# Optimization experiments

Hardware: AMD Instinct MI355X
Metric: run time of the kernel (lower is better)

Reference implementation:

```python
import jax, jax.numpy as jnp
import numpy as np

N = 100_000      # nodes
E = 1_600_000    # edges (avg degree 16)
H = 128          # hidden_channels == num_node_features
L = 6            # SAGEConv layers (third=True)
G = 128          # graphs in batch (for global_mean_pool)
C = 10           # num_classes
EPS = 1e-5       # BatchNorm eps


def setup_inputs() -> dict:
    key = jax.random.key(0)
    ks = jax.random.split(key, 8)
    s = 1.0 / np.sqrt(H)
    x = jax.random.normal(ks[0], (N, H), jnp.float32)
    edge_index = jax.random.randint(ks[1], (2, E), 0, N, dtype=jnp.int32)
    batch = jnp.sort(jax.random.randint(ks[2], (N,), 0, G, dtype=jnp.int32))
    return {
        "x": x,
        "edge_index": edge_index,
        "batch": batch,
        "Wl": jax.random.normal(ks[3], (L, H, H), jnp.float32) * s,  # neighbor lin
        "bl": jnp.zeros((L, H), jnp.float32),
        "Wr": jax.random.normal(ks[4], (L, H, H), jnp.float32) * s,  # root lin (no bias)
        "gamma": jnp.ones((L, H), jnp.float32),
        "beta": jnp.zeros((L, H), jnp.float32),
        "lin_W": jax.random.normal(ks[5], (H, C), jnp.float32) * s,
        "lin_b": jnp.zeros((C,), jnp.float32),
    }


def reference(x, edge_index, batch, Wl, bl, Wr, gamma, beta, lin_W, lin_b):
    src, dst = edge_index[0], edge_index[1]
    n = x.shape[0]
    # in-degree for mean aggregation (constant across layers)
    deg = jax.ops.segment_sum(jnp.ones((src.shape[0],), x.dtype), dst, num_segments=n)
    inv_deg = jnp.where(deg > 0, 1.0 / deg, 0.0)[:, None]  # [n,1]

    for l in range(Wl.shape[0]):
        # SAGEConv: lin_l(mean_{j->i} x_j) + lin_r(x_i)
        agg = jax.ops.segment_sum(x[src], dst, num_segments=n) * inv_deg  # [n,H]
        h = agg @ Wl[l] + bl[l] + x @ Wr[l]
        # BatchNorm1d (training-style batch stats, biased variance)
        mu = jnp.mean(h, axis=0)
        var = jnp.mean((h - mu) ** 2, axis=0)
        h = (h - mu) * jax.lax.rsqrt(var + EPS) * gamma[l] + beta[l]
        x = jax.nn.relu(h)

    # global_mean_pool over graph ids
    cnt = jax.ops.segment_sum(jnp.ones((n,), x.dtype), batch, num_segments=G)
    pooled = jax.ops.segment_sum(x, batch, num_segments=G) / jnp.maximum(cnt, 1.0)[:, None]
    # dropout(p=0.5) is identity in eval mode
    return pooled @ lin_W + lin_b  # [G, C]
```

## Files before the change

kernel.cpp:

```cpp
#include <hip/hip_runtime.h>
#include <hip/hip_bf16.h>

#define N_NODES 100000
#define N_EDGES 1600000
#define HDIM    128
#define NLAYER  6
#define NGRAPH  128
#define NCLASS  10
#define BN_EPS  1e-5f

#define POOL_SPLIT 16

#define NBUCK   196
#define BSH     9
#define KC_BLOCKS 250
#define KC_CHUNK  6400
#define LCOL_CAP  10240

#define GBM 128
#define NBLK_G ((N_NODES + GBM - 1) / GBM)

typedef __attribute__((ext_vector_type(8))) short short8v;
typedef __attribute__((ext_vector_type(4))) float f32x4;
typedef __attribute__((ext_vector_type(2))) float f32x2;
typedef __attribute__((ext_vector_type(4))) int int4v;
typedef __attribute__((ext_vector_type(2))) int int2v;

__device__ __forceinline__ float b2f(unsigned short h) {
    return __uint_as_float(((unsigned int)h) << 16);
}
__device__ __forceinline__ unsigned short f2b(float f) {
    unsigned int u = __float_as_uint(f);
    u += 0x7FFF + ((u >> 16) & 1);
    return (unsigned short)(u >> 16);
}
__device__ __forceinline__ void gl_lds16(const void* g, void* l) {
    __builtin_amdgcn_global_load_lds((const __attribute__((address_space(1))) unsigned int*)g,
                                     (__attribute__((address_space(3))) unsigned int*)l,
                                     16, 0, 0);
}
__device__ __forceinline__ short8v bn_pack(short8v v, float4 scA, float4 scB,
                                           float4 shA, float4 shB) {
    short8v o;
    o[0] = (short)f2b(fmaxf(0.f, b2f((unsigned short)v[0]) * scA.x + shA.x));
    o[1] = (short)f2b(fmaxf(0.f, b2f((unsigned short)v[1]) * scA.y + shA.y));
    o[2] = (short)f2b(fmaxf(0.f, b2f((unsigned short)v[2]) * scA.z + shA.z));
    o[3] = (short)f2b(fmaxf(0.f, b2f((unsigned short)v[3]) * scA.w + shA.w));
    o[4] = (short)f2b(fmaxf(0.f, b2f((unsigned short)v[4]) * scB.x + shB.x));
    o[5] = (short)f2b(fmaxf(0.f, b2f((unsigned short)v[5]) * scB.y + shB.y));
    o[6] = (short)f2b(fmaxf(0.f, b2f((unsigned short)v[6]) * scB.z + shB.z));
    o[7] = (short)f2b(fmaxf(0.f, b2f((unsigned short)v[7]) * scB.w + shB.w));
    return o;
}


__global__ void __launch_bounds__(256) k_hist(const int* __restrict__ dst,
                                              int* __restrict__ bcnt) {
    __shared__ int h[NBUCK];
    for (int i = threadIdx.x; i < NBUCK; i += 256) h[i] = 0;
    __syncthreads();
    const int4v* d4 = (const int4v*)dst;
    int base = blockIdx.x * (KC_CHUNK / 4);
    for (int i = threadIdx.x; i < KC_CHUNK / 4; i += 256) {
        int4v d = __builtin_nontemporal_load(d4 + base + i);
        atomicAdd(&h[d[0] >> BSH], 1);
        atomicAdd(&h[d[1] >> BSH], 1);
        atomicAdd(&h[d[2] >> BSH], 1);
        atomicAdd(&h[d[3] >> BSH], 1);
    }
    __syncthreads();
    for (int i = threadIdx.x; i < NBUCK; i += 256)
        if (h[i]) atomicAdd(&bcnt[i], h[i]);
}

__global__ void k_bscan(const int* __restrict__ bcnt, int* __restrict__ boff,
                        int* __restrict__ bcur, int* __restrict__ row_off) {
    if (threadIdx.x == 0 && blockIdx.x == 0) {
        int acc = 0;
        for (int i = 0; i < NBUCK; ++i) {
            boff[i] = acc; bcur[i] = acc; acc += bcnt[i];
        }
        boff[NBUCK] = acc;
        row_off[N_NODES] = N_EDGES;
    }
}

__global__ void __launch_bounds__(256) k_part(const int* __restrict__ src,
                                              const int* __restrict__ dst,
                                              int* __restrict__ bcur,
                                              int2v* __restrict__ P) {
    __shared__ int h[NBUCK];
    __shared__ int gbase[NBUCK];
    for (int i = threadIdx.x; i < NBUCK; i += 256) h[i] = 0;
    __syncthreads();
    const int4v* d4 = (const int4v*)dst;
    const int4v* s4 = (const int4v*)src;
    const int base = blockIdx.x * (KC_CHUNK / 4);
    for (int i = threadIdx.x; i < KC_CHUNK / 4; i += 256) {
        int4v d = __builtin_nontemporal_load(d4 + base + i);
        atomicAdd(&h[d[0] >> BSH], 1);
        atomicAdd(&h[d[1] >> BSH], 1);
        atomicAdd(&h[d[2] >> BSH], 1);
        atomicAdd(&h[d[3] >> BSH], 1);
    }
    __syncthreads();
    for (int i = threadIdx.x; i < NBUCK; i += 256) {
        int c = h[i];
        gbase[i] = c ? atomicAdd(&bcur[i], c) : 0;
        h[i] = 0;
    }
    __syncthreads();
    for (int i = threadIdx.x; i < KC_CHUNK / 4; i += 256) {
        int4v d = __builtin_nontemporal_load(d4 + base + i);
        int4v s = __builtin_nontemporal_load(s4 + base + i);
#pragma unroll
        for (int k = 0; k < 4; ++k) {
            int b = d[k] >> BSH;
            int pos = gbase[b] + atomicAdd(&h[b], 1);
            int2v pr; pr[0] = s[k]; pr[1] = d[k];
            P[pos] = pr;
        }
    }
}

__global__ void __launch_bounds__(1024) k_bucket(const int2v* __restrict__ P,
                                                 const int* __restrict__ boff,
                                                 int* __restrict__ row_off,
                                                 int* __restrict__ col) {
    __shared__ int ldeg[512];
    __shared__ int lcur[512];
    __shared__ int lcol[LCOL_CAP];
    const int tid = threadIdx.x;
    const int b = blockIdx.x;
    const int pbeg = boff[b], pend = boff[b + 1];
    const int nE = pend - pbeg;
    const int n0 = b << BSH;
    if (tid < 512) ldeg[tid] = 0;
    __syncthreads();
    for (int i = tid; i < nE; i += 1024) {
        int2v pr = P[pbeg + i];
        atomicAdd(&ldeg[pr[1] - n0], 1);
    }
    __syncthreads();
    int myd = (tid < 512) ? ldeg[tid] : 0;
    for (int off = 1; off < 512; off <<= 1) {
        int t = 0;
        if (tid < 512 && tid >= off) t = ldeg[tid - off];
        __syncthreads();
        if (tid < 512) ldeg[tid] += t;
        __syncthreads();
    }
    if (tid < 512) {
        int excl = ldeg[tid] - myd;
        lcur[tid] = excl;
        int node = n0 + tid;
        if (node < N_NODES) row_off[node] = pbeg + excl;
    }
    __syncthreads();
    for (int i = tid; i < nE; i += 1024) {
        int2v pr = P[pbeg + i];
        int pos = atomicAdd(&lcur[pr[1] - n0], 1);
        if (pos < LCOL_CAP) lcol[pos] = pr[0];
    }
    __syncthreads();
    for (int i = tid; i < nE; i += 1024) col[pbeg + i] = lcol[i];
}


__global__ void __launch_bounds__(256) k_cvt_x(const float* __restrict__ x,
                                               unsigned short* __restrict__ Xb,
                                               unsigned int* __restrict__ X8) {
    int idx = blockIdx.x * 256 + threadIdx.x;
    f32x4 v = __builtin_nontemporal_load(((const f32x4*)x) + idx);
    ushort4 o = { f2b(v[0]), f2b(v[1]), f2b(v[2]), f2b(v[3]) };
    ((ushort4*)Xb)[idx] = o;
    unsigned int d = 0;
    d = __builtin_amdgcn_cvt_pk_fp8_f32(v[0], v[1], d, false);
    d = __builtin_amdgcn_cvt_pk_fp8_f32(v[2], v[3], d, true);
    X8[idx] = d;
}

__global__ void __launch_bounds__(256) k_cvt_w(const float* __restrict__ Wl,
                                               const float* __restrict__ Wr,
                                               unsigned short* __restrict__ Wtb) {
    int idx = blockIdx.x * 256 + threadIdx.x;
    int kk = idx & 255;
    int n  = (idx >> 8) & 127;
    int l  = idx >> 15;
    float v = (kk < HDIM) ? Wl[l * HDIM * HDIM + kk * HDIM + n]
                          : Wr[l * HDIM * HDIM + (kk - HDIM) * HDIM + n];
    Wtb[idx] = f2b(v);
}

__global__ void __launch_bounds__(256) k_bnx8(const unsigned short* __restrict__ Hb,
                                              const float* __restrict__ scsh,
                                              int2v* __restrict__ X8) {
    int idx = blockIdx.x * 256 + threadIdx.x;
    int c8 = (idx & 15) * 8;
    short8v v = ((const short8v*)Hb)[idx];
    float f[8];
#pragma unroll
    for (int j = 0; j < 8; ++j)
        f[j] = fmaxf(0.f, b2f((unsigned short)v[j]) * scsh[c8 + j] + scsh[HDIM + c8 + j]);
    unsigned int d0 = 0, d1 = 0;
    d0 = __builtin_amdgcn_cvt_pk_fp8_f32(f[0], f[1], d0, false);
    d0 = __builtin_amdgcn_cvt_pk_fp8_f32(f[2], f[3], d0, true);
    d1 = __builtin_amdgcn_cvt_pk_fp8_f32(f[4], f[5], d1, false);
    d1 = __builtin_amdgcn_cvt_pk_fp8_f32(f[6], f[7], d1, true);
    int2v o; o[0] = (int)d0; o[1] = (int)d1;
    X8[idx] = o;
}


template<bool BN>
__global__ void __launch_bounds__(512) k_fused(const unsigned char* __restrict__ X8,
                                               const unsigned short* __restrict__ Hprev,
                                               const float* __restrict__ scsh,
                                               const int* __restrict__ row_off,
                                               const int* __restrict__ col,
                                               const unsigned short* __restrict__ Wtb,
                                               const float* __restrict__ bl,
                                               unsigned short* __restrict__ Hb,
                                               float* __restrict__ pstat) {
    __shared__ __align__(16) char smem[32768];
    __shared__ int sro[129];
    const int tid  = threadIdx.x;
    const int bm   = blockIdx.x * GBM;
    const int wv   = tid >> 6;
    const int lane = tid & 63;
    const int li   = lane & 15, hi = lane >> 4;
    const int wm   = wv & 1, wn = wv >> 1;
    const int rr   = tid >> 2, sk = tid & 3;
    const int swz  = ((sk ^ ((rr >> 1) & 3)) << 4);

    gl_lds16((const char*)(Wtb + (size_t)rr * 256) + swz, smem + 16384 + wv * 1024);

    int* lcol = (int*)smem;
    if (tid <= 128) {
        int ii = bm + tid; if (ii > N_NODES) ii = N_NODES;
        sro[tid] = row_off[ii];
    }
    __syncthreads();
    const int s0 = sro[0];
    const int nEb = sro[128] - s0;
    const bool fits = (nEb <= 4096);
    if (fits) for (int i = tid; i < nEb; i += 512) lcol[i] = col[s0 + i];
    __syncthreads();

    const int s = sro[rr] - s0, e = sro[rr + 1] - s0;
    const int* cp = fits ? lcol : (col + s0);
    const int c32 = sk * 32;
    f32x2 a2[16] = {};
    auto accum16 = [&](int4v v, int base) {
#pragma unroll
        for (int q = 0; q < 4; ++q) {
            unsigned int w = (unsigned int)v[q];
            a2[base + 2 * q]     += __builtin_amdgcn_cvt_pk_f32_fp8(w, false);
            a2[base + 2 * q + 1] += __builtin_amdgcn_cvt_pk_f32_fp8(w, true);
        }
    };
    int p = s;
    for (; p + 4 <= e; p += 4) {
        int nbx[4];
#pragma unroll
        for (int j = 0; j < 4; ++j) nbx[j] = cp[p + j];
        int4v v0[4], v1[4];
#pragma unroll
        for (int j = 0; j < 4; ++j) {
            const unsigned char* rowp = X8 + (size_t)nbx[j] * HDIM + c32;
            v0[j] = *(const int4v*)rowp;
            v1[j] = *(const int4v*)(rowp + 16);
        }
#pragma unroll
        for (int j = 0; j < 4; ++j) { accum16(v0[j], 0); accum16(v1[j], 8); }
    }
    for (; p < e; ++p) {
        const unsigned char* rowp = X8 + (size_t)cp[p] * HDIM + c32;
        accum16(*(const int4v*)rowp, 0);
        accum16(*(const int4v*)(rowp + 16), 8);
    }
    const float wgt = (e > s) ? 1.0f / (float)(e - s) : 0.f;
    short8v aggout[4];
#pragma unroll
    for (int j = 0; j < 4; ++j)
#pragma unroll
        for (int t = 0; t < 8; ++t)
            aggout[j][t] = (short)f2b(a2[j * 4 + (t >> 1)][t & 1] * wgt);

    __syncthreads();
    if (sk == 0) {
#pragma unroll
        for (int j = 0; j < 4; ++j)
            *(short8v*)(smem + rr * 64 + ((j ^ ((rr >> 1) & 3)) << 4)) = aggout[j];
    }
    __syncthreads();

    f32x4 acc[4][2] = {};
    int buf = 0;
    for (int step = 0; step < 8; ++step) {
        char* curA = smem + buf * 8192;
        char* curW = smem + 16384 + buf * 8192;
        char* nxtA = smem + (buf ^ 1) * 8192;
        const int ns = step + 1;
        short8v rv;
        int c0 = 0;
        bool regstage = false;
        if (step < 7) {
            gl_lds16((const char*)(Wtb + (size_t)rr * 256 + ns * 32) + swz,
                     smem + 16384 + (buf ^ 1) * 8192 + wv * 1024);
            if (ns >= 4) {
                regstage = true;
                c0 = (ns - 4) * 32 + sk * 8;
                int row = bm + rr; if (row >= N_NODES) row = N_NODES - 1;
                rv = *(const short8v*)(Hprev + (size_t)row * HDIM + c0);
            }
        }

        short8v afr[4], bfr[2];
#pragma unroll
        for (int m = 0; m < 4; ++m) {
            int r = wm * 64 + m * 16 + li;
            afr[m] = *(const short8v*)(curA + r * 64 + ((hi ^ ((r >> 1) & 3)) << 4));
        }
#pragma unroll
        for (int nf = 0; nf < 2; ++nf) {
            int n = wn * 32 + nf * 16 + li;
            bfr[nf] = *(const short8v*)(curW + n * 64 + ((hi ^ ((n >> 1) & 3)) << 4));
        }
#pragma unroll
        for (int m = 0; m < 4; ++m)
#pragma unroll
            for (int nf = 0; nf < 2; ++nf)
                acc[m][nf] = __builtin_amdgcn_mfma_f32_16x16x32_bf16(afr[m], bfr[nf],
                                                                     acc[m][nf], 0, 0, 0);

        if (step < 7) {
            if (ns < 4) {
                if (sk == ns) {
#pragma unroll
                    for (int j = 0; j < 4; ++j)
                        *(short8v*)(nxtA + rr * 64 + ((j ^ ((rr >> 1) & 3)) << 4)) = aggout[j];
                }
            } else {
                short8v ov;
                if (BN) {
                    float4 scA = *(const float4*)&scsh[c0];
                    float4 scB = *(const float4*)&scsh[c0 + 4];
                    float4 shA = *(const float4*)&scsh[HDIM + c0];
                    float4 shB = *(const float4*)&scsh[HDIM + c0 + 4];
                    ov = bn_pack(rv, scA, scB, shA, shB);
                } else {
                    ov = rv;
                }
                *(short8v*)(nxtA + rr * 64 + swz) = ov;
            }
        }
        __syncthreads();
        buf ^= 1;
    }

    float* st = (float*)smem;
#pragma unroll
    for (int nf = 0; nf < 2; ++nf) {
        int c = wn * 32 + nf * 16 + li;
        float bb = bl[c];
        float ls = 0.f, lq = 0.f;
#pragma unroll
        for (int m = 0; m < 4; ++m) {
            int row0 = bm + wm * 64 + m * 16 + hi * 4;
#pragma unroll
            for (int j = 0; j < 4; ++j) {
                int row = row0 + j;
                if (row < N_NODES) {
                    float v = acc[m][nf][j] + bb;
                    Hb[(size_t)row * HDIM + c] = f2b(v);
                    ls += v; lq += v * v;
                }
            }
        }
        ls += __shfl_xor(ls, 16); ls += __shfl_xor(ls, 32);
        lq += __shfl_xor(lq, 16); lq += __shfl_xor(lq, 32);
        if (hi == 0) {
            st[wv * 128 + c] = ls;
            st[1024 + wv * 128 + c] = lq;
        }
    }
    __syncthreads();
    if (tid < 128) {
        int w0 = (tid >> 5) * 2;
        float s2 = st[w0 * 128 + tid] + st[(w0 + 1) * 128 + tid];
        pstat[blockIdx.x * 256 + tid] = s2;
    } else if (tid < 256) {
        int c = tid - 128;
        int w0 = (c >> 5) * 2;
        float q = st[1024 + w0 * 128 + c] + st[1024 + (w0 + 1) * 128 + c];
        pstat[blockIdx.x * 256 + tid] = q;
    }
}


__global__ void __launch_bounds__(256) k_red1(const float* __restrict__ pstat,
                                              float* __restrict__ red32) {
    int c = threadIdx.x, b = blockIdx.x;
    float s = 0.f;
    for (int r = b; r < NBLK_G; r += 32) s += pstat[r * 256 + c];
    red32[b * 256 + c] = s;
}

__global__ void __launch_bounds__(128) k_stats_final(const float* __restrict__ red32,
                                                     const float* __restrict__ gamma,
                                                     const float* __restrict__ beta,
                                                     float* __restrict__ scsh) {
    int c = threadIdx.x;
    float s = 0.f, q = 0.f;
    for (int r = 0; r < 32; ++r) { s += red32[r * 256 + c]; q += red32[r * 256 + 128 + c]; }
    float mu = s / (float)N_NODES;
    float var = q / (float)N_NODES - mu * mu;
    float rs = rsqrtf(var + BN_EPS);
    float sc = gamma[c] * rs;
    scsh[c] = sc;
    scsh[HDIM + c] = beta[c] - mu * sc;
}


__global__ void k_gbound(const int* __restrict__ batch, int* __restrict__ gb) {
    int t = blockIdx.x * 64 + threadIdx.x;
    if (t > NGRAPH) return;
    int lo = 0, hi = N_NODES;
    while (lo < hi) { int mid = (lo + hi) >> 1; if (batch[mid] < t) lo = mid + 1; else hi = mid; }
    gb[t] = lo;
}

__global__ void __launch_bounds__(128) k_pool_part(const unsigned short* __restrict__ Hb,
                                                   const float* __restrict__ scsh,
                                                   const int* __restrict__ gb,
                                                   float* __restrict__ ppart) {
    int g = blockIdx.x, sp = blockIdx.y;
    int c = threadIdx.x;
    float sc = scsh[c], sh = scsh[HDIM + c];
    int s = gb[g], e = gb[g + 1];
    float acc = 0.f;
    for (int i = s + sp; i < e; i += POOL_SPLIT)
        acc += fmaxf(0.f, b2f(Hb[(size_t)i * HDIM + c]) * sc + sh);
    ppart[(g * POOL_SPLIT + sp) * HDIM + c] = acc;
}

__global__ void __launch_bounds__(128) k_pool_final(const int* __restrict__ gb,
                                                    const float* __restrict__ ppart,
                                                    float* __restrict__ pooled) {
    int g = blockIdx.x, c = threadIdx.x;
    float s = 0.f;
    for (int sp = 0; sp < POOL_SPLIT; ++sp) s += ppart[(g * POOL_SPLIT + sp) * HDIM + c];
    int cnt = gb[g + 1] - gb[g]; if (cnt < 1) cnt = 1;
    pooled[g * HDIM + c] = s / (float)cnt;
}

__global__ void __launch_bounds__(128) k_lin(const float* __restrict__ pooled,
                                             const float* __restrict__ W,
                                             const float* __restrict__ bvec,
                                             float* __restrict__ out) {
    __shared__ float p[HDIM];
    int g = blockIdx.x, t = threadIdx.x;
    p[t] = pooled[g * HDIM + t];
    __syncthreads();
    if (t < NCLASS) {
        float acc = bvec[t];
        for (int k = 0; k < HDIM; ++k) acc += p[k] * W[k * NCLASS + t];
        out[g * NCLASS + t] = acc;
    }
}


extern "C" void kernel_launch(void* const* d_in, const int* in_sizes, int n_in,
                              void* d_out, int out_size, void* d_ws, size_t ws_size,
                              hipStream_t stream) {
    const float* x     = (const float*)d_in[0];
    const int*   eidx  = (const int*)d_in[1];
    const int*   batch = (const int*)d_in[2];
    const float* Wl    = (const float*)d_in[3];
    const float* bl    = (const float*)d_in[4];
    const float* Wr    = (const float*)d_in[5];
    const float* gamma = (const float*)d_in[6];
    const float* beta  = (const float*)d_in[7];
    const float* linW  = (const float*)d_in[8];
    const float* linb  = (const float*)d_in[9];
    float* out = (float*)d_out;

    const int* src = eidx;
    const int* dst = eidx + N_EDGES;

    char* p = (char*)d_ws;
    auto alloc = [&](size_t bytes) { char* r = p; p += (bytes + 255) & ~(size_t)255; return r; };
    unsigned short* Xb   = (unsigned short*)alloc((size_t)N_NODES * HDIM * 2);
    unsigned char*  X8   = (unsigned char*)alloc((size_t)N_NODES * HDIM);
    unsigned short* HbA  = (unsigned short*)alloc((size_t)N_NODES * HDIM * 2);
    unsigned short* HbB  = (unsigned short*)alloc((size_t)N_NODES * HDIM * 2);
    unsigned short* Wtb  = (unsigned short*)alloc((size_t)NLAYER * 2 * HDIM * HDIM * 2);
    int*   row_off = (int*)alloc((N_NODES + 2) * 4);
    int*   col     = (int*)alloc((size_t)N_EDGES * 4);
    int2v* P       = (int2v*)alloc((size_t)N_EDGES * 8);
    int*   bcnt    = (int*)alloc(NBUCK * 4);
    int*   boff    = (int*)alloc((NBUCK + 1) * 4);
    int*   bcur    = (int*)alloc(NBUCK * 4);
    int*   gb      = (int*)alloc((NGRAPH + 2) * 4);
    float* pstat   = (float*)alloc((size_t)NBLK_G * 256 * 4);
    float* red32   = (float*)alloc(32 * 256 * 4);
    float* scsh    = (float*)alloc(2 * HDIM * 4);
    float* ppart   = (float*)alloc((size_t)NGRAPH * POOL_SPLIT * HDIM * 4);
    float* pooled  = (float*)alloc(NGRAPH * HDIM * 4);

    hipMemsetAsync(bcnt, 0, NBUCK * sizeof(int), stream);
    k_hist<<<KC_BLOCKS, 256, 0, stream>>>(dst, bcnt);
    k_bscan<<<1, 64, 0, stream>>>(bcnt, boff, bcur, row_off);
    k_part<<<KC_BLOCKS, 256, 0, stream>>>(src, dst, bcur, P);
    k_bucket<<<NBUCK, 1024, 0, stream>>>(P, boff, row_off, col);

    k_cvt_x<<<N_NODES * HDIM / 4 / 256, 256, 0, stream>>>(x, Xb, (unsigned int*)X8);
    k_cvt_w<<<NLAYER * 2 * HDIM * HDIM / 256, 256, 0, stream>>>(Wl, Wr, Wtb);
    k_gbound<<<3, 64, 0, stream>>>(batch, gb);

    k_fused<false><<<NBLK_G, 512, 0, stream>>>(X8, Xb, scsh, row_off, col,
                                               Wtb, bl, HbA, pstat);
    k_red1<<<32, 256, 0, stream>>>(pstat, red32);
    k_stats_final<<<1, 128, 0, stream>>>(red32, gamma, beta, scsh);

    unsigned short* Hcur = HbA;
    for (int l = 1; l < NLAYER; ++l) {
        unsigned short* Hout = (l & 1) ? HbB : HbA;
        k_bnx8<<<N_NODES * HDIM / 8 / 256, 256, 0, stream>>>(Hcur, scsh, (int2v*)X8);
        k_fused<true><<<NBLK_G, 512, 0, stream>>>(
            X8, Hcur, scsh, row_off, col, Wtb + (size_t)l * 2 * HDIM * HDIM,
            bl + (size_t)l * HDIM, Hout, pstat);
        k_red1<<<32, 256, 0, stream>>>(pstat, red32);
        k_stats_final<<<1, 128, 0, stream>>>(red32, gamma + (size_t)l * HDIM,
                                             beta + (size_t)l * HDIM, scsh);
        Hcur = Hout;
    }

    k_pool_part<<<dim3(NGRAPH, POOL_SPLIT), 128, 0, stream>>>(Hcur, scsh, gb, ppart);
    k_pool_final<<<NGRAPH, 128, 0, stream>>>(gb, ppart, pooled);
    k_lin<<<NGRAPH, 128, 0, stream>>>(pooled, linW, linb, out);
}
```

Measured before the change: 557.2 us.

## Double fused SAGE kernel block to 1024 threads with 8 lanes per row gather

The fused gather+GEMM kernel now launches 1024 threads per 128-row tile. Each row's neighbor gather is split across 8 lanes of 16 bytes instead of 4 lanes of 32 bytes, with an 8-deep load batch, and the MFMA work is split across 16 waves (2x2 fragments each). The aim is more memory-level parallelism in the irregular fp8 gather and better latency hiding. In exchange, each wave does less MFMA work, block-wide syncs cost more, register pressure under the 1024-thread launch bound rises, and occupancy per CU may drop.

```diff
diff --git a/kernel.cpp b/kernel.cpp
--- a/kernel.cpp
+++ b/kernel.cpp
@@ -213,15 +213,15 @@
 
 
 template<bool BN>
-__global__ void __launch_bounds__(512) k_fused(const unsigned char* __restrict__ X8,
-                                               const unsigned short* __restrict__ Hprev,
-                                               const float* __restrict__ scsh,
-                                               const int* __restrict__ row_off,
-                                               const int* __restrict__ col,
-                                               const unsigned short* __restrict__ Wtb,
-                                               const float* __restrict__ bl,
-                                               unsigned short* __restrict__ Hb,
-                                               float* __restrict__ pstat) {
+__global__ void __launch_bounds__(1024) k_fused(const unsigned char* __restrict__ X8,
+                                                const unsigned short* __restrict__ Hprev,
+                                                const float* __restrict__ scsh,
+                                                const int* __restrict__ row_off,
+                                                const int* __restrict__ col,
+                                                const unsigned short* __restrict__ Wtb,
+                                                const float* __restrict__ bl,
+                                                unsigned short* __restrict__ Hb,
+                                                float* __restrict__ pstat) {
     __shared__ __align__(16) char smem[32768];
     __shared__ int sro[129];
     const int tid  = threadIdx.x;
@@ -229,11 +229,13 @@
     const int wv   = tid >> 6;
     const int lane = tid & 63;
     const int li   = lane & 15, hi = lane >> 4;
-    const int wm   = wv & 1, wn = wv >> 1;
-    const int rr   = tid >> 2, sk = tid & 3;
-    const int swz  = ((sk ^ ((rr >> 1) & 3)) << 4);
-
-    gl_lds16((const char*)(Wtb + (size_t)rr * 256) + swz, smem + 16384 + wv * 1024);
+    const int wm   = wv & 3, wn = wv >> 2;
+
+    if (tid < 512) {
+        int rw = tid >> 2, skw = tid & 3;
+        gl_lds16((const char*)(Wtb + (size_t)rw * 256) + (((skw ^ ((rw >> 1) & 3)) & 3) << 4),
+                 smem + 16384 + wv * 1024);
+    }
 
     int* lcol = (int*)smem;
     if (tid <= 128) {
@@ -244,58 +246,69 @@
     const int s0 = sro[0];
     const int nEb = sro[128] - s0;
     const bool fits = (nEb <= 4096);
-    if (fits) for (int i = tid; i < nEb; i += 512) lcol[i] = col[s0 + i];
-    __syncthreads();
-
-    const int s = sro[rr] - s0, e = sro[rr + 1] - s0;
+    if (fits) for (int i = tid; i < nEb; i += 1024) lcol[i] = col[s0 + i];
+    __syncthreads();
+
+    const int grr = tid >> 3, gsk = tid & 7;
+    const int s = sro[grr] - s0, e = sro[grr + 1] - s0;
     const int* cp = fits ? lcol : (col + s0);
-    const int c32 = sk * 32;
-    f32x2 a2[16] = {};
-    auto accum16 = [&](int4v v, int base) {
+    const int c16 = gsk * 16;
+    f32x2 a2[8] = {};
+    auto accum = [&](int4v v) {
 #pragma unroll
         for (int q = 0; q < 4; ++q) {
             unsigned int w = (unsigned int)v[q];
-            a2[base + 2 * q]     += __builtin_amdgcn_cvt_pk_f32_fp8(w, false);
-            a2[base + 2 * q + 1] += __builtin_amdgcn_cvt_pk_f32_fp8(w, true);
+            a2[2 * q]     += __builtin_amdgcn_cvt_pk_f32_fp8(w, false);
+            a2[2 * q + 1] += __builtin_amdgcn_cvt_pk_f32_fp8(w, true);
         }
     };
     int p = s;
-    for (; p + 4 <= e; p += 4) {
+    for (; p + 8 <= e; p += 8) {
+        int nbx[8];
+#pragma unroll
+        for (int j = 0; j < 8; ++j) nbx[j] = cp[p + j];
+        int4v v[8];
+#pragma unroll
+        for (int j = 0; j < 8; ++j)
+            v[j] = *(const int4v*)(X8 + (size_t)nbx[j] * HDIM + c16);
+#pragma unroll
+        for (int j = 0; j < 8; ++j) accum(v[j]);
+    }
+    if (p + 4 <= e) {
         int nbx[4];
 #pragma unroll
         for (int j = 0; j < 4; ++j) nbx[j] = cp[p + j];
-        int4v v0[4], v1[4];
-#pragma unroll
-        for (int j = 0; j < 4; ++j) {
-            const unsigned char* rowp = X8 + (size_t)nbx[j] * HDIM + c32;
-            v0[j] = *(const int4v*)rowp;
-            v1[j] = *(const int4v*)(rowp + 16);
-        }
-#pragma unroll
-        for (int j = 0; j < 4; ++j) { accum16(v0[j], 0); accum16(v1[j], 8); }
+        int4v v[4];
+#pragma unroll
+        for (int j = 0; j < 4; ++j)
+            v[j] = *(const int4v*)(X8 + (size_t)nbx[j] * HDIM + c16);
+#pragma unroll
+        for (int j = 0; j < 4; ++j) accum(v[j]);
+        p += 4;
     }
     for (; p < e; ++p) {
-        const unsigned char* rowp = X8 + (size_t)cp[p] * HDIM + c32;
-        accum16(*(const int4v*)rowp, 0);
-        accum16(*(const int4v*)(rowp + 16), 8);
+        int4v v0 = *(const int4v*)(X8 + (size_t)cp[p] * HDIM + c16);
+        accum(v0);
     }
     const float wgt = (e > s) ? 1.0f / (float)(e - s) : 0.f;
-    short8v aggout[4];
-#pragma unroll
-    for (int j = 0; j < 4; ++j)
-#pragma unroll
-        for (int t = 0; t < 8; ++t)
-            aggout[j][t] = (short)f2b(a2[j * 4 + (t >> 1)][t & 1] * wgt);
-
-    __syncthreads();
-    if (sk == 0) {
-#pragma unroll
-        for (int j = 0; j < 4; ++j)
-            *(short8v*)(smem + rr * 64 + ((j ^ ((rr >> 1) & 3)) << 4)) = aggout[j];
-    }
-    __syncthreads();
-
-    f32x4 acc[4][2] = {};
+    short8v o0, o1;
+#pragma unroll
+    for (int t = 0; t < 8; ++t) o0[t] = (short)f2b(a2[t >> 1][t & 1] * wgt);
+#pragma unroll
+    for (int t = 0; t < 8; ++t) o1[t] = (short)f2b(a2[4 + (t >> 1)][t & 1] * wgt);
+
+    const int jstep = gsk >> 1;
+    const int sl0 = 2 * (gsk & 1);
+    const int gswz = (grr >> 1) & 3;
+
+    __syncthreads();
+    if (jstep == 0) {
+        *(short8v*)(smem + grr * 64 + (((sl0)     ^ gswz) << 4)) = o0;
+        *(short8v*)(smem + grr * 64 + (((sl0 + 1) ^ gswz) << 4)) = o1;
+    }
+    __syncthreads();
+
+    f32x4 acc[2][2] = {};
     int buf = 0;
     for (int step = 0; step < 8; ++step) {
         char* curA = smem + buf * 8192;
@@ -306,20 +319,24 @@
         int c0 = 0;
         bool regstage = false;
         if (step < 7) {
-            gl_lds16((const char*)(Wtb + (size_t)rr * 256 + ns * 32) + swz,
-                     smem + 16384 + (buf ^ 1) * 8192 + wv * 1024);
-            if (ns >= 4) {
+            if (tid < 512) {
+                int rw = tid >> 2, skw = tid & 3;
+                gl_lds16((const char*)(Wtb + (size_t)rw * 256 + ns * 32) +
+                             (((skw ^ ((rw >> 1) & 3)) & 3) << 4),
+                         smem + 16384 + (buf ^ 1) * 8192 + wv * 1024);
+            }
+            if (ns >= 4 && gsk < 4) {
                 regstage = true;
-                c0 = (ns - 4) * 32 + sk * 8;
-                int row = bm + rr; if (row >= N_NODES) row = N_NODES - 1;
+                c0 = (ns - 4) * 32 + gsk * 8;
+                int row = bm + grr; if (row >= N_NODES) row = N_NODES - 1;
                 rv = *(const short8v*)(Hprev + (size_t)row * HDIM + c0);
             }
         }
 
-        short8v afr[4], bfr[2];
-#pragma unroll
-        for (int m = 0; m < 4; ++m) {
-            int r = wm * 64 + m * 16 + li;
+        short8v afr[2], bfr[2];
+#pragma unroll
+        for (int m = 0; m < 2; ++m) {
+            int r = wm * 32 + m * 16 + li;
             afr[m] = *(const short8v*)(curA + r * 64 + ((hi ^ ((r >> 1) & 3)) << 4));
         }
 #pragma unroll
@@ -328,7 +345,7 @@
             bfr[nf] = *(const short8v*)(curW + n * 64 + ((hi ^ ((n >> 1) & 3)) << 4));
         }
 #pragma unroll
-        for (int m = 0; m < 4; ++m)
+        for (int m = 0; m < 2; ++m)
 #pragma unroll
             for (int nf = 0; nf < 2; ++nf)
                 acc[m][nf] = __builtin_amdgcn_mfma_f32_16x16x32_bf16(afr[m], bfr[nf],
@@ -336,12 +353,11 @@
 
         if (step < 7) {
             if (ns < 4) {
-                if (sk == ns) {
-#pragma unroll
-                    for (int j = 0; j < 4; ++j)
-                        *(short8v*)(nxtA + rr * 64 + ((j ^ ((rr >> 1) & 3)) << 4)) = aggout[j];
+                if (jstep == ns) {
+                    *(short8v*)(nxtA + grr * 64 + (((sl0)     ^ gswz) << 4)) = o0;
+                    *(short8v*)(nxtA + grr * 64 + (((sl0 + 1) ^ gswz) << 4)) = o1;
                 }
-            } else {
+            } else if (regstage) {
                 short8v ov;
                 if (BN) {
                     float4 scA = *(const float4*)&scsh[c0];
@@ -352,7 +368,7 @@
                 } else {
                     ov = rv;
                 }
-                *(short8v*)(nxtA + rr * 64 + swz) = ov;
+                *(short8v*)(nxtA + grr * 64 + ((gsk ^ gswz) << 4)) = ov;
             }
         }
         __syncthreads();
@@ -366,8 +382,8 @@
         float bb = bl[c];
         float ls = 0.f, lq = 0.f;
 #pragma unroll
-        for (int m = 0; m < 4; ++m) {
-            int row0 = bm + wm * 64 + m * 16 + hi * 4;
+        for (int m = 0; m < 2; ++m) {
+            int row0 = bm + wm * 32 + m * 16 + hi * 4;
 #pragma unroll
             for (int j = 0; j < 4; ++j) {
                 int row = row0 + j;
@@ -382,18 +398,20 @@
         lq += __shfl_xor(lq, 16); lq += __shfl_xor(lq, 32);
         if (hi == 0) {
             st[wv * 128 + c] = ls;
-            st[1024 + wv * 128 + c] = lq;
+            st[2048 + wv * 128 + c] = lq;
         }
     }
     __syncthreads();
     if (tid < 128) {
-        int w0 = (tid >> 5) * 2;
-        float s2 = st[w0 * 128 + tid] + st[(w0 + 1) * 128 + tid];
+        int w0 = 4 * (tid >> 5);
+        float s2 = st[w0 * 128 + tid] + st[(w0 + 1) * 128 + tid]
+                 + st[(w0 + 2) * 128 + tid] + st[(w0 + 3) * 128 + tid];
         pstat[blockIdx.x * 256 + tid] = s2;
     } else if (tid < 256) {
         int c = tid - 128;
-        int w0 = (c >> 5) * 2;
-        float q = st[1024 + w0 * 128 + c] + st[1024 + (w0 + 1) * 128 + c];
+        int w0 = 4 * (c >> 5);
+        float q = st[2048 + w0 * 128 + c] + st[2048 + (w0 + 1) * 128 + c]
+                + st[2048 + (w0 + 2) * 128 + c] + st[2048 + (w0 + 3) * 128 + c];
         pstat[blockIdx.x * 256 + tid] = q;
     }
 }
@@ -519,8 +537,8 @@
     k_cvt_w<<<NLAYER * 2 * HDIM * HDIM / 256, 256, 0, stream>>>(Wl, Wr, Wtb);
     k_gbound<<<3, 64, 0, stream>>>(batch, gb);
 
-    k_fused<false><<<NBLK_G, 512, 0, stream>>>(X8, Xb, scsh, row_off, col,
-                                               Wtb, bl, HbA, pstat);
+    k_fused<false><<<NBLK_G, 1024, 0, stream>>>(X8, Xb, scsh, row_off, col,
+                                                Wtb, bl, HbA, pstat);
     k_red1<<<32, 256, 0, stream>>>(pstat, red32);
     k_stats_final<<<1, 128, 0, stream>>>(red32, gamma, beta, scsh);
 
@@ -528,7 +546,7 @@
     for (int l = 1; l < NLAYER; ++l) {
         unsigned short* Hout = (l & 1) ? HbB : HbA;
         k_bnx8<<<N_NODES * HDIM / 8 / 256, 256, 0, stream>>>(Hcur, scsh, (int2v*)X8);
-        k_fused<true><<<NBLK_G, 512, 0, stream>>>(
+        k_fused<true><<<NBLK_G, 1024, 0, stream>>>(
             X8, Hcur, scsh, row_off, col, Wtb + (size_t)l * 2 * HDIM * HDIM,
             bl + (size_t)l * HDIM, Hout, pstat);
         k_red1<<<32, 256, 0, stream>>>(pstat, red32);
```

Measured after the change: 657.1 us. 1.18x slower.
